# Kernel tuning notes

Hardware: AMD Instinct MI355X
Metric: run time of the kernel (lower is better)

## Reference

```python
import jax, jax.numpy as jnp
import numpy as np

N_CLASSES = 64
MAX_ITER = 50
EPS = 1e-4


def _sqdist(x, y):
    # squared euclidean distances [n, m]
    d = (x * x).sum(-1)[:, None] + (y * y).sum(-1)[None, :] - 2.0 * (x @ y.T)
    return jnp.maximum(d, 0.0)


def setup_inputs() -> dict:
    key = jax.random.key(0)
    k1, k2, k3 = jax.random.split(key, 3)
    return {
        "feat_s": jax.random.normal(k1, (1600, 1024), jnp.float32),
        "y_s": jax.random.randint(k2, (1600,), 0, N_CLASSES),
        "feat_q": jax.random.normal(k3, (4096, 1024), jnp.float32),
    }


def _prototypes(feat_s, y_s):
    sums = jax.ops.segment_sum(feat_s, y_s, num_segments=N_CLASSES)
    cnt = jax.ops.segment_sum(jnp.ones((feat_s.shape[0],), feat_s.dtype), y_s, num_segments=N_CLASSES)
    return sums / jnp.maximum(cnt, 1.0)[:, None]


def _affinity(feat):
    n = feat.shape[0]
    k = max(1, int(np.log2(n)))  # self-tuning neighborhood size
    dist = jnp.sqrt(_sqdist(feat, feat))
    _, nn_idx = jax.lax.top_k(-dist, k + 1)  # ascending distance order
    rows = jnp.arange(n)
    sigma = dist[rows, nn_idx[:, k]] + 1e-8  # k-th neighbor distance
    nbrs = nn_idx[:, 1:]  # [n, k], drop self
    w = jnp.exp(-jnp.take_along_axis(dist, nbrs, axis=1) / (sigma[:, None] * sigma[nbrs]))
    W = jnp.zeros((n, n), feat.dtype).at[rows[:, None], nbrs].set(w)
    W = (W + W.T) / 2.0
    D_inv = 1.0 / (W.sum(1) + 1e-8)
    return W, D_inv


def _mm_iterations(feat, prototypes, W, D_inv, lam):
    a = _sqdist(feat, prototypes)  # [n, C]
    coef = (lam * D_inv)[:, None]

    def step(y):
        return jax.nn.softmax(-a + coef * (W @ y), axis=1)

    y0 = jax.nn.softmax(-a, axis=1)

    def cond(s):
        y, y_new, i = s
        return (i < MAX_ITER) & (jnp.max(jnp.abs(y_new - y)) >= EPS)

    def body(s):
        y, y_new, i = s
        return (y_new, step(y_new), i + 1)

    y, _, _ = jax.lax.while_loop(cond, body, (y0, step(y0), 0))
    return y


def reference(feat_s, y_s, feat_q):
    protos = _prototypes(feat_s, y_s)
    W, D_inv = _affinity(feat_q)
    d2 = _sqdist(feat_q, protos).min(1)  # squared min distance to prototypes
    d = jnp.sqrt(d2)
    lam = jnp.exp(-d2 / (2.0 * jnp.median(d) ** 2 + 1e-8))
    y = _mm_iterations(feat_q, protos, W, D_inv, lam)
    return jnp.argmax(y, axis=1)
```

## Files before the change

kernel.cpp:

```cpp
#include <hip/hip_runtime.h>
#include <hip/hip_cooperative_groups.h>
#include <cfloat>
#include <cmath>

#define N_Q 4096
#define N_S 1600
#define DIM 1024
#define N_C 64
#define KNN 12
#define MAX_ITER 50
#define EPS_CONV 1e-4f
#define NBLK 256
#define ADJ_CAP 96
#define CHK 256
#define DPAD 40

typedef _Float16 h8 __attribute__((ext_vector_type(8)));
typedef float    f4 __attribute__((ext_vector_type(4)));

__device__ __forceinline__ float wave_max64(float v){
  #pragma unroll
  for (int o = 32; o; o >>= 1) v = fmaxf(v, __shfl_xor(v, o, 64));
  return v;
}
__device__ __forceinline__ float wave_sum64(float v){
  #pragma unroll
  for (int o = 32; o; o >>= 1) v += __shfl_xor(v, o, 64);
  return v;
}
__device__ __forceinline__ float wave_min64(float v){
  #pragma unroll
  for (int o = 32; o; o >>= 1) v = fminf(v, __shfl_xor(v, o, 64));
  return v;
}

__device__ __forceinline__ float aload(const float* p){
  return __hip_atomic_load(p, __ATOMIC_RELAXED, __HIP_MEMORY_SCOPE_AGENT);
}
__device__ __forceinline__ void astore(float* p, float v){
  __hip_atomic_store(p, v, __ATOMIC_RELAXED, __HIP_MEMORY_SCOPE_AGENT);
}
__device__ __forceinline__ int aloadi(const int* p){
  return __hip_atomic_load(p, __ATOMIC_RELAXED, __HIP_MEMORY_SCOPE_AGENT);
}
__device__ __forceinline__ void astorei(int* p, int v){
  __hip_atomic_store(p, v, __ATOMIC_RELAXED, __HIP_MEMORY_SCOPE_AGENT);
}
__device__ __forceinline__ unsigned long long aload64(const unsigned long long* p){
  return __hip_atomic_load(p, __ATOMIC_RELAXED, __HIP_MEMORY_SCOPE_AGENT);
}
__device__ __forceinline__ void astore64(unsigned long long* p, unsigned long long v){
  __hip_atomic_store(p, v, __ATOMIC_RELAXED, __HIP_MEMORY_SCOPE_AGENT);
}

__global__ __launch_bounds__(256) void setup_kernel(
    const float* __restrict__ fs, const int* __restrict__ ys,
    float* __restrict__ Pt, float* __restrict__ pn,
    const float* __restrict__ X, float* __restrict__ qn,
    _Float16* __restrict__ Xh, _Float16* __restrict__ Xl)
{
  __shared__ union {
    struct {
      int   list[N_S];
      int   pref[256];
      int   lcount;
      float red[256];
    } p;
    float red[256];
  } S;

  const int t = threadIdx.x;

  if (blockIdx.x < N_C){
    const int c = blockIdx.x;
    int loc[7]; int cnt = 0;
    const int base = t * 7;
    #pragma unroll
    for (int u = 0; u < 7; u++){
      const int i = base + u;
      if (i < N_S && ys[i] == c) loc[cnt++] = i;
    }
    S.p.pref[t] = cnt;
    __syncthreads();
    for (int off = 1; off < 256; off <<= 1){
      int v = (t >= off) ? S.p.pref[t - off] : 0;
      __syncthreads();
      S.p.pref[t] += v;
      __syncthreads();
    }
    const int start = S.p.pref[t] - cnt;
    for (int u = 0; u < cnt; u++) S.p.list[start + u] = loc[u];
    if (t == 255) S.p.lcount = S.p.pref[255];
    __syncthreads();

    const int n = S.p.lcount;
    float a0 = 0.f, a1 = 0.f, a2 = 0.f, a3 = 0.f;
    for (int m = 0; m < n; m++){
      const float* r = fs + (size_t)S.p.list[m] * DIM;
      a0 += r[t]; a1 += r[t + 256]; a2 += r[t + 512]; a3 += r[t + 768];
    }
    const float inv = 1.0f / fmaxf((float)n, 1.0f);
    const float v0 = a0*inv, v1 = a1*inv, v2 = a2*inv, v3 = a3*inv;
    Pt[(t      )*N_C + c] = v0;
    Pt[(t + 256)*N_C + c] = v1;
    Pt[(t + 512)*N_C + c] = v2;
    Pt[(t + 768)*N_C + c] = v3;
    S.p.red[t] = v0*v0 + v1*v1 + v2*v2 + v3*v3;
    __syncthreads();
    for (int o = 128; o; o >>= 1){ if (t < o) S.p.red[t] += S.p.red[t + o]; __syncthreads(); }
    if (t == 0) pn[c] = S.p.red[0];
  } else {
    const int i = blockIdx.x - N_C;
    const float* r = X + (size_t)i * DIM;
    const float v0 = r[t], v1 = r[t+256], v2 = r[t+512], v3 = r[t+768];
    const size_t b = (size_t)i * DIM;
    _Float16 h0 = (_Float16)v0, h1 = (_Float16)v1, h2 = (_Float16)v2, h3 = (_Float16)v3;
    Xh[b + t      ] = h0; Xl[b + t      ] = (_Float16)(v0 - (float)h0);
    Xh[b + t + 256] = h1; Xl[b + t + 256] = (_Float16)(v1 - (float)h1);
    Xh[b + t + 512] = h2; Xl[b + t + 512] = (_Float16)(v2 - (float)h2);
    Xh[b + t + 768] = h3; Xl[b + t + 768] = (_Float16)(v3 - (float)h3);
    S.red[t] = v0*v0 + v1*v1 + v2*v2 + v3*v3;
    __syncthreads();
    for (int o = 128; o; o >>= 1){ if (t < o) S.red[t] += S.red[t + o]; __syncthreads(); }
    if (t == 0) qn[i] = S.red[0];
  }
}

__global__ __launch_bounds__(256, 2) void dist_mfma(
    const _Float16* __restrict__ Xh, const _Float16* __restrict__ Xl,
    const float* __restrict__ qn, float* __restrict__ Dq)
{
  __shared__ __align__(16) _Float16 As[2][128][DPAD];
  __shared__ __align__(16) _Float16 Bs[2][256][DPAD];

  const int t = threadIdx.x, w = t >> 6, l = t & 63;
  const int lb  = blockIdx.x;
  const int xcd = lb & 7, k = lb >> 3;
  const int bxs = xcd * 2 + (k >> 5);
  const int bys = k & 31;
  const int bi0 = bys * 128, bj0 = bxs * 256;
  const int j0w = w * 64;
  const int fr = l & 15;
  const int kq = (l >> 4) * 8;

  const int arow = t >> 1;
  const int aseg = (t & 1) * 16;
  const int brow = t;

  f4 acc[8][4];
  #pragma unroll
  for (int a = 0; a < 8; a++)
    #pragma unroll
    for (int b = 0; b < 4; b++) acc[a][b] = (f4){0.f, 0.f, 0.f, 0.f};

  const size_t abase = (size_t)(bi0 + arow) * DIM + aseg;
  const size_t bbase = (size_t)(bj0 + brow) * DIM;

  #pragma unroll 1
  for (int k0 = 0; k0 < DIM; k0 += 32){
    h8 va0 = *(const h8*)(Xh + abase + k0);
    h8 va1 = *(const h8*)(Xh + abase + k0 + 8);
    h8 vb0 = *(const h8*)(Xl + abase + k0);
    h8 vb1 = *(const h8*)(Xl + abase + k0 + 8);
    h8 vc0 = *(const h8*)(Xh + bbase + k0);
    h8 vc1 = *(const h8*)(Xh + bbase + k0 + 8);
    h8 vc2 = *(const h8*)(Xh + bbase + k0 + 16);
    h8 vc3 = *(const h8*)(Xh + bbase + k0 + 24);
    h8 vd0 = *(const h8*)(Xl + bbase + k0);
    h8 vd1 = *(const h8*)(Xl + bbase + k0 + 8);
    h8 vd2 = *(const h8*)(Xl + bbase + k0 + 16);
    h8 vd3 = *(const h8*)(Xl + bbase + k0 + 24);
    __syncthreads();
    *(h8*)&As[0][arow][aseg    ] = va0;
    *(h8*)&As[0][arow][aseg + 8] = va1;
    *(h8*)&As[1][arow][aseg    ] = vb0;
    *(h8*)&As[1][arow][aseg + 8] = vb1;
    *(h8*)&Bs[0][brow][0 ] = vc0;
    *(h8*)&Bs[0][brow][8 ] = vc1;
    *(h8*)&Bs[0][brow][16] = vc2;
    *(h8*)&Bs[0][brow][24] = vc3;
    *(h8*)&Bs[1][brow][0 ] = vd0;
    *(h8*)&Bs[1][brow][8 ] = vd1;
    *(h8*)&Bs[1][brow][16] = vd2;
    *(h8*)&Bs[1][brow][24] = vd3;
    __syncthreads();

    h8 ah[8], al[8];
    #pragma unroll
    for (int sm = 0; sm < 8; sm++){
      ah[sm] = *(const h8*)&As[0][sm * 16 + fr][kq];
      al[sm] = *(const h8*)&As[1][sm * 16 + fr][kq];
    }
    #pragma unroll
    for (int sn = 0; sn < 4; sn++){
      h8 bh = *(const h8*)&Bs[0][j0w + sn * 16 + fr][kq];
      h8 bl = *(const h8*)&Bs[1][j0w + sn * 16 + fr][kq];
      #pragma unroll
      for (int sm = 0; sm < 8; sm++){
        acc[sm][sn] = __builtin_amdgcn_mfma_f32_16x16x32_f16(ah[sm], bh, acc[sm][sn], 0, 0, 0);
        acc[sm][sn] = __builtin_amdgcn_mfma_f32_16x16x32_f16(ah[sm], bl, acc[sm][sn], 0, 0, 0);
        acc[sm][sn] = __builtin_amdgcn_mfma_f32_16x16x32_f16(al[sm], bh, acc[sm][sn], 0, 0, 0);
      }
    }
  }

  const int cr = (l >> 4) * 4;
  const int cc = l & 15;
  #pragma unroll
  for (int sm = 0; sm < 8; sm++){
    #pragma unroll
    for (int r = 0; r < 4; r++){
      const int row = bi0 + sm * 16 + cr + r;
      const float qi = qn[row];
      float* dstrow = &Dq[(size_t)row * N_Q];
      #pragma unroll
      for (int sn = 0; sn < 4; sn++){
        const int col = bj0 + j0w + sn * 16 + cc;
        float d2 = qi + qn[col] - 2.0f * acc[sm][sn][r];
        dstrow[col] = sqrtf(fmaxf(d2, 0.f));
      }
    }
  }
}

__global__ __launch_bounds__(256) void topk_kernel(
    const float* __restrict__ Dq, int* __restrict__ nbr,
    float* __restrict__ dnbr, float* __restrict__ sigma)
{
  const int i = blockIdx.x, t = threadIdx.x;
  const int lane = t & 63, w = t >> 6;
  const float* row = Dq + (size_t)i * N_Q;
  float r[16];
  #pragma unroll
  for (int u = 0; u < 16; u++) r[u] = row[t + u * 256];

  __shared__ float cvf[4 * (KNN + 1)];
  __shared__ int   cif[4 * (KNN + 1)];

  float keepv = FLT_MAX; int keepi = 0x7fffffff;
  for (int s = 0; s < KNN + 1; s++){
    float best = FLT_MAX; int bj = 0x7fffffff;
    #pragma unroll
    for (int u = 0; u < 16; u++){
      float v = r[u];
      if (v < best){ best = v; bj = t + u * 256; }
    }
    #pragma unroll
    for (int o = 32; o; o >>= 1){
      float ov = __shfl_xor(best, o, 64); int oj = __shfl_xor(bj, o, 64);
      if (ov < best || (ov == best && oj < bj)){ best = ov; bj = oj; }
    }
    if (lane == s){ keepv = best; keepi = bj; }
    if ((bj & 255) == t) r[bj >> 8] = FLT_MAX;
  }
  if (lane < KNN + 1){ cvf[w * (KNN + 1) + lane] = keepv; cif[w * (KNN + 1) + lane] = keepi; }
  __syncthreads();

  if (w == 0){
    float mv = FLT_MAX; int mi = 0x7fffffff;
    if (lane < 4 * (KNN + 1)){ mv = cvf[lane]; mi = cif[lane]; }
    for (int s = 0; s < KNN + 1; s++){
      float best = mv; int bj = mi;
      #pragma unroll
      for (int o = 32; o; o >>= 1){
        float ov = __shfl_xor(best, o, 64); int oj = __shfl_xor(bj, o, 64);
        if (ov < best || (ov == best && oj < bj)){ best = ov; bj = oj; }
      }
      if (lane == 0){
        if (s >= 1){ nbr[i*KNN + s - 1] = bj; dnbr[i*KNN + s - 1] = best; }
        if (s == KNN) sigma[i] = best + 1e-8f;
      }
      if (mi == bj) mv = FLT_MAX;
    }
  }
}

__device__ __forceinline__ void gbar_leader(int* garr, int* gcnt, int* gen, int target){
  const int g = blockIdx.x >> 4;
  int old = __hip_atomic_fetch_add(&garr[g * 32], 1, __ATOMIC_RELAXED, __HIP_MEMORY_SCOPE_AGENT);
  if ((old & 15) == 15){
    int o2 = __hip_atomic_fetch_add(gcnt, 1, __ATOMIC_RELAXED, __HIP_MEMORY_SCOPE_AGENT);
    if ((o2 & 15) == 15)
      __hip_atomic_fetch_add(gen, 1, __ATOMIC_RELAXED, __HIP_MEMORY_SCOPE_AGENT);
  }
  while (__hip_atomic_load(gen, __ATOMIC_RELAXED, __HIP_MEMORY_SCOPE_AGENT) < target)
    __builtin_amdgcn_s_sleep(1);
}

__device__ __forceinline__ void pbar_wave0(
    unsigned long long* pslot, int ph, int* sdm, float* sdelta_sh, int lane)
{
  const int par = ph & 1;
  unsigned long long* base = pslot + (size_t)par * NBLK;
  if (lane == 0){
    int myd = sdm[par]; sdm[par] = 0;
    unsigned long long pack =
        ((unsigned long long)(unsigned int)myd << 32) | (unsigned int)ph;
    __builtin_amdgcn_s_waitcnt(0);
    astore64(&base[blockIdx.x], pack);
  }
  int mx;
  while (1){
    unsigned long long v0 = aload64(&base[lane      ]);
    unsigned long long v1 = aload64(&base[lane +  64]);
    unsigned long long v2 = aload64(&base[lane + 128]);
    unsigned long long v3 = aload64(&base[lane + 192]);
    int f0 = (int)(unsigned int)v0, f1 = (int)(unsigned int)v1;
    int f2 = (int)(unsigned int)v2, f3 = (int)(unsigned int)v3;
    int mn = f0 < f1 ? f0 : f1;
    mn = f2 < mn ? f2 : mn;
    mn = f3 < mn ? f3 : mn;
    if (__all(mn >= ph)){
      int d0 = (int)(v0 >> 32), d1 = (int)(v1 >> 32);
      int d2 = (int)(v2 >> 32), d3 = (int)(v3 >> 32);
      mx = d0 > d1 ? d0 : d1;
      mx = d2 > mx ? d2 : mx;
      mx = d3 > mx ? d3 : mx;
      break;
    }
    __builtin_amdgcn_s_sleep(1);
  }
  #pragma unroll
  for (int o = 32; o; o >>= 1){ int ox = __shfl_xor(mx, o, 64); mx = ox > mx ? ox : mx; }
  if (lane == 0) *sdelta_sh = __int_as_float(mx);
}

template<int K>
__device__ __forceinline__ void chunk_fma(
    const float* __restrict__ src, const int2* adj, int gbase, int lane,
    float& s0, float& s1, float& s2, float& s3,
    float& s4, float& s5, float& s6, float& s7)
{
  float yv[K][8], wv[K][8];
  #pragma unroll
  for (int g = 0; g < K; g++){
    #pragma unroll
    for (int u = 0; u < 8; u++){
      int2 a = adj[(gbase + g) * 8 + u];
      wv[g][u] = __int_as_float(a.y);
      yv[g][u] = aload(&src[a.x + lane]);
    }
  }
  #pragma unroll
  for (int g = 0; g < K; g++){
    s0 = fmaf(wv[g][0], yv[g][0], s0);
    s1 = fmaf(wv[g][1], yv[g][1], s1);
    s2 = fmaf(wv[g][2], yv[g][2], s2);
    s3 = fmaf(wv[g][3], yv[g][3], s3);
    s4 = fmaf(wv[g][4], yv[g][4], s4);
    s5 = fmaf(wv[g][5], yv[g][5], s5);
    s6 = fmaf(wv[g][6], yv[g][6], s6);
    s7 = fmaf(wv[g][7], yv[g][7], s7);
  }
}

__device__ __forceinline__ float spmv_row(
    const float* __restrict__ src, const int2* adj,
    const int* __restrict__ colA, const float* __restrict__ wA,
    int p0, int p1v, int lane)
{
  const int deg  = p1v - p0;
  const int ncap = deg < ADJ_CAP ? deg : ADJ_CAP;
  const int nfull = ncap & ~7;
  const int ng = nfull >> 3;
  float s0=0.f,s1=0.f,s2=0.f,s3=0.f,s4=0.f,s5=0.f,s6=0.f,s7=0.f;

  int g = 0;
  #pragma unroll 1
  for (; g + 4 <= ng; g += 4){
    chunk_fma<4>(src, adj, g, lane, s0,s1,s2,s3,s4,s5,s6,s7);
  }
  {
    const int left = ng - g;
    if (left == 3)      chunk_fma<3>(src, adj, g, lane, s0,s1,s2,s3,s4,s5,s6,s7);
    else if (left == 2) chunk_fma<2>(src, adj, g, lane, s0,s1,s2,s3,s4,s5,s6,s7);
    else if (left == 1) chunk_fma<1>(src, adj, g, lane, s0,s1,s2,s3,s4,s5,s6,s7);
  }

  if (deg > ADJ_CAP){
    int qg = p0 + ADJ_CAP;
    for (; qg + 8 <= p1v; qg += 8){
      s0 = fmaf(wA[qg    ], aload(&src[colA[qg    ] + lane]), s0);
      s1 = fmaf(wA[qg + 1], aload(&src[colA[qg + 1] + lane]), s1);
      s2 = fmaf(wA[qg + 2], aload(&src[colA[qg + 2] + lane]), s2);
      s3 = fmaf(wA[qg + 3], aload(&src[colA[qg + 3] + lane]), s3);
      s4 = fmaf(wA[qg + 4], aload(&src[colA[qg + 4] + lane]), s4);
      s5 = fmaf(wA[qg + 5], aload(&src[colA[qg + 5] + lane]), s5);
      s6 = fmaf(wA[qg + 6], aload(&src[colA[qg + 6] + lane]), s6);
      s7 = fmaf(wA[qg + 7], aload(&src[colA[qg + 7] + lane]), s7);
    }
    for (; qg < p1v; qg++)
      s0 = fmaf(wA[qg], aload(&src[colA[qg] + lane]), s0);
  } else {
    const int rem = deg - nfull;
    if (rem > 0){
      float yr[7], wr[7];
      #pragma unroll
      for (int u = 0; u < 7; u++){
        if (u < rem){
          int2 a = adj[nfull + u];
          wr[u] = __int_as_float(a.y);
          yr[u] = aload(&src[a.x + lane]);
        }
      }
      #pragma unroll
      for (int u = 0; u < 7; u++)
        if (u < rem) s0 = fmaf(wr[u], yr[u], s0);
    }
  }
  return ((s0+s1)+(s2+s3)) + ((s4+s5)+(s6+s7));
}

__global__ __launch_bounds__(1024, 4) void tail_loop(
    const float* __restrict__ Xq, const float* __restrict__ Pt,
    const float* __restrict__ pn, const float* __restrict__ qn,
    const int* __restrict__ nbr, const float* __restrict__ dnbr,
    const float* __restrict__ sigma,
    float* d2min, float* denom, float* wh,
    float* rowsum, int* indeg, int* rowptr, int* fillc,
    int* colA, float* wA, float* buf0, float* buf1,
    unsigned long long* pslot,
    int* gcnt, int* gen, int* garr, int* __restrict__ out)
{
  __shared__ int   sdm[2];
  __shared__ float sdelta;
  __shared__ union {
    float pchunk[CHK * N_C];
    struct {
      int   ipart[1024];
      int   hist[1024];
      float cand[4096];
      int   candn, b1s, b2s;
    } s;
  } U;
  __shared__ int2  adjL[16 * ADJ_CAP];

  const int tid  = threadIdx.x;
  const int lane = tid & 63;
  const int wv   = tid >> 6;
  const int row  = blockIdx.x * 16 + wv;
  if (tid == 0){ sdm[0] = 0; sdm[1] = 0; }

  const float* xr = Xq + (size_t)row * DIM;
  const f4*    xr4 = (const f4*)xr;
  float dp[8];
  #pragma unroll
  for (int u = 0; u < 8; u++) dp[u] = 0.f;

  for (int f0 = 0; f0 < DIM; f0 += CHK){
    const f4* srcv = (const f4*)(Pt + (size_t)f0 * N_C);
    f4* dstv = (f4*)U.pchunk;
    #pragma unroll
    for (int u = 0; u < 4; u++) dstv[tid + u * 1024] = srcv[tid + u * 1024];
    __syncthreads();
    #pragma unroll 1
    for (int f = 0; f < CHK; f += 8){
      const f4 xa = xr4[(f0 + f) >> 2];
      const f4 xb = xr4[((f0 + f) >> 2) + 1];
      const float* pc = U.pchunk + f * N_C + lane;
      dp[0] = fmaf(xa[0], pc[0      ], dp[0]);
      dp[1] = fmaf(xa[1], pc[N_C    ], dp[1]);
      dp[2] = fmaf(xa[2], pc[N_C * 2], dp[2]);
      dp[3] = fmaf(xa[3], pc[N_C * 3], dp[3]);
      dp[4] = fmaf(xb[0], pc[N_C * 4], dp[4]);
      dp[5] = fmaf(xb[1], pc[N_C * 5], dp[5]);
      dp[6] = fmaf(xb[2], pc[N_C * 6], dp[6]);
      dp[7] = fmaf(xb[3], pc[N_C * 7], dp[7]);
    }
    __syncthreads();
  }
  const float dot = ((dp[0]+dp[1])+(dp[2]+dp[3])) + ((dp[4]+dp[5])+(dp[6]+dp[7]));
  const float av  = fmaxf(qn[row] + pn[lane] - 2.0f * dot, 0.0f);
  const float d2m = wave_min64(av);
  if (lane == 0) astore(&d2min[row], d2m);

  const int e = blockIdx.x * 1024 + tid;
  if (e < N_Q * KNN){
    const int i = e / KNN;
    const int j = nbr[e];
    float wgt = 0.5f * expf(-dnbr[e] / (sigma[i] * sigma[j]));
    astore(&wh[e], wgt);
    atomicAdd(&rowsum[i], wgt);
    atomicAdd(&rowsum[j], wgt);
    atomicAdd(&indeg[j], 1);
  }

  __syncthreads();
  if (tid == 0) gbar_leader(garr, gcnt, gen, 1);
  __syncthreads();

  float xv = -av;
  float m = wave_max64(xv), ee = expf(xv - m), ss = wave_sum64(ee);
  float prev = ee / ss;
  astore(&buf0[row * N_C + lane], prev);

  if (blockIdx.x == 0){
    int* ipart = U.s.ipart;
    const int base = tid * 4;
    int c0 = aloadi(&indeg[base]),     c1 = aloadi(&indeg[base + 1]);
    int c2 = aloadi(&indeg[base + 2]), c3 = aloadi(&indeg[base + 3]);
    const int s4 = c0 + c1 + c2 + c3;
    ipart[tid] = s4;
    __syncthreads();
    for (int off = 1; off < 1024; off <<= 1){
      int v = (tid >= off) ? ipart[tid - off] : 0;
      __syncthreads();
      ipart[tid] += v;
      __syncthreads();
    }
    int run = ipart[tid] - s4;
    astorei(&rowptr[base    ], KNN * (base    ) + run); run += c0;
    astorei(&rowptr[base + 1], KNN * (base + 1) + run); run += c1;
    astorei(&rowptr[base + 2], KNN * (base + 2) + run); run += c2;
    astorei(&rowptr[base + 3], KNN * (base + 3) + run);
    if (tid == 1023) astorei(&rowptr[N_Q], KNN * N_Q + ipart[1023]);
  }
  if (blockIdx.x == 1){
    int*   hist = U.s.hist;
    float* cand = U.s.cand;
    const int base = tid * 4;
    float dv[4];
    #pragma unroll
    for (int u = 0; u < 4; u++) dv[u] = sqrtf(aload(&d2min[base + u]));
    float mn = fminf(fminf(dv[0], dv[1]), fminf(dv[2], dv[3]));
    float mx = fmaxf(fmaxf(dv[0], dv[1]), fmaxf(dv[2], dv[3]));
    mn = wave_min64(mn); mx = wave_max64(mx);
    if (lane == 0){ cand[wv] = mn; cand[wv + 16] = mx; }
    __syncthreads();
    if (tid == 0){
      float a = cand[0], b = cand[16];
      for (int k = 1; k < 16; k++){ a = fminf(a, cand[k]); b = fmaxf(b, cand[16 + k]); }
      cand[32] = a; cand[33] = b;
    }
    __syncthreads();
    mn = cand[32]; mx = cand[33];
    const float rng = mx - mn;
    const float scale = (rng > 0.f) ? (1024.0f / rng) : 0.f;
    hist[tid] = 0;
    __syncthreads();
    int bidx[4];
    #pragma unroll
    for (int u = 0; u < 4; u++){
      int b = (int)((dv[u] - mn) * scale);
      b = b < 0 ? 0 : (b > 1023 ? 1023 : b);
      bidx[u] = b;
      atomicAdd(&hist[b], 1);
    }
    __syncthreads();
    for (int off = 1; off < 1024; off <<= 1){
      int v = (tid >= off) ? hist[tid - off] : 0;
      __syncthreads();
      hist[tid] += v;
      __syncthreads();
    }
    if (hist[tid] >= 2048 && (tid == 0 || hist[tid - 1] < 2048)) U.s.b1s = tid;
    if (hist[tid] >= 2049 && (tid == 0 || hist[tid - 1] < 2049)) U.s.b2s = tid;
    if (tid == 0) U.s.candn = 0;
    __syncthreads();
    const int b1 = U.s.b1s, b2 = U.s.b2s;
    const int cntBefore = (b1 > 0) ? hist[b1 - 1] : 0;
    #pragma unroll
    for (int u = 0; u < 4; u++){
      if (bidx[u] >= b1 && bidx[u] <= b2){
        int pos = atomicAdd(&U.s.candn, 1);
        cand[pos] = dv[u];
      }
    }
    __syncthreads();
    const int mcnt = U.s.candn;
    int P = 2; while (P < mcnt) P <<= 1;
    for (int i2 = mcnt + tid; i2 < P; i2 += 1024) cand[i2] = FLT_MAX;
    __syncthreads();
    for (int k = 2; k <= P; k <<= 1){
      for (int st = k >> 1; st > 0; st >>= 1){
        for (int i2 = tid; i2 < P; i2 += 1024){
          int j2 = i2 ^ st;
          if (j2 > i2){
            float a2 = cand[i2], b3 = cand[j2];
            bool up = ((i2 & k) == 0);
            if (up ? (a2 > b3) : (a2 < b3)){ cand[i2] = b3; cand[j2] = a2; }
          }
        }
        __syncthreads();
      }
    }
    if (tid == 0){
      float v1 = cand[2047 - cntBefore], v2 = cand[2048 - cntBefore];
      float med = 0.5f * (v1 + v2);
      astore(denom, 2.0f * med * med + 1e-8f);
    }
  }

  __syncthreads();
  if (tid == 0) gbar_leader(garr, gcnt, gen, 2);
  __syncthreads();

  if (e < N_Q * KNN){
    const int i = e / KNN, tt = e % KNN;
    const int j = nbr[e];
    const float wgt = aload(&wh[e]);
    const int p = aloadi(&rowptr[i]) + tt;
    colA[p] = j * N_C; wA[p] = wgt;
    const int q = aloadi(&rowptr[j]) + KNN + atomicAdd(&fillc[j], 1);
    colA[q] = i * N_C; wA[q] = wgt;
  }
  const float cf = expf(-d2m / aload(denom)) / (aload(&rowsum[row]) + 1e-8f);
  const int p0  = aloadi(&rowptr[row]);
  const int p1v = aloadi(&rowptr[row + 1]);

  __builtin_amdgcn_fence(__ATOMIC_RELEASE, "agent");
  __syncthreads();
  if (tid == 0) gbar_leader(garr, gcnt, gen, 3);
  __syncthreads();
  __builtin_amdgcn_fence(__ATOMIC_ACQUIRE, "agent");

  {
    const int deg  = p1v - p0;
    const int ncap = deg < ADJ_CAP ? deg : ADJ_CAP;
    for (int u = lane; u < ncap; u += 64)
      adjL[wv * ADJ_CAP + u] = make_int2(colA[p0 + u], __float_as_int(wA[p0 + u]));
  }
  __syncthreads();
  const int2* adj = adjL + wv * ADJ_CAP;

  float cur;
  {
    float sum = spmv_row(buf0, adj, colA, wA, p0, p1v, lane);
    float xv2 = -av + cf * sum;
    float mm = wave_max64(xv2), e2 = expf(xv2 - mm), ss2 = wave_sum64(e2);
    cur = e2 / ss2;
    astore(&buf1[row * N_C + lane], cur);
  }
  float dm = wave_max64(fabsf(cur - prev));
  if (lane == 0) atomicMax(&sdm[1], __float_as_int(dm));
  __syncthreads();
  if (wv == 0) pbar_wave0(pslot, 1, sdm, &sdelta, lane);
  __syncthreads();
  float delta = sdelta;

  int par = 1;
  for (int t = 0;; t++){
    if (t >= MAX_ITER || delta < EPS_CONV) break;
    const float* src = par ? buf1 : buf0;
    float*       dst = par ? buf0 : buf1;
    float sum = spmv_row(src, adj, colA, wA, p0, p1v, lane);
    float xv2 = -av + cf * sum;
    float mm = wave_max64(xv2), e2 = expf(xv2 - mm), ss2 = wave_sum64(e2);
    float nxt = e2 / ss2;
    astore(&dst[row * N_C + lane], nxt);
    const int ph = t + 2;
    dm = wave_max64(fabsf(nxt - cur));
    if (lane == 0) atomicMax(&sdm[ph & 1], __float_as_int(dm));
    __syncthreads();
    if (wv == 0) pbar_wave0(pslot, ph, sdm, &sdelta, lane);
    __syncthreads();
    delta = sdelta;
    prev = cur; cur = nxt; par ^= 1;
  }

  float bv = prev; int bi = lane;
  #pragma unroll
  for (int o = 32; o; o >>= 1){
    float ov = __shfl_xor(bv, o, 64); int oi = __shfl_xor(bi, o, 64);
    if (ov > bv || (ov == bv && oi < bi)){ bv = ov; bi = oi; }
  }
  if (lane == 0) out[row] = bi;
}

extern "C" void kernel_launch(void* const* d_in, const int* in_sizes, int n_in,
                              void* d_out, int out_size, void* d_ws, size_t ws_size,
                              hipStream_t stream)
{
  const float* feat_s = (const float*)d_in[0];
  const int*   y_s    = (const int*)d_in[1];
  const float* feat_q = (const float*)d_in[2];
  int* out = (int*)d_out;

  char* wp = (char*)d_ws;
  auto alloc = [&](size_t bytes) -> char* {
    char* p = wp;
    wp += (bytes + 255) & ~(size_t)255;
    return p;
  };
  float*     Dq  = (float*)alloc((size_t)N_Q * N_Q * 4);
  _Float16*  Xh  = (_Float16*)alloc((size_t)N_Q * DIM * 2);
  _Float16*  Xl  = (_Float16*)alloc((size_t)N_Q * DIM * 2);
  float* Pt     = (float*)alloc((size_t)DIM * N_C * 4);
  float* pn     = (float*)alloc(N_C * 4);
  float* qn     = (float*)alloc(N_Q * 4);
  float* d2min  = (float*)alloc(N_Q * 4);
  float* denom  = (float*)alloc(256);
  int*   nbr    = (int*)alloc((size_t)N_Q * KNN * 4);
  float* dnbr   = (float*)alloc((size_t)N_Q * KNN * 4);
  float* sigma  = (float*)alloc(N_Q * 4);
  float* wh     = (float*)alloc((size_t)N_Q * KNN * 4);
  int*   rowptr = (int*)alloc((N_Q + 1) * 4);
  int*   colA   = (int*)alloc((size_t)2 * N_Q * KNN * 4);
  float* wA     = (float*)alloc((size_t)2 * N_Q * KNN * 4);
  float* buf0   = (float*)alloc((size_t)N_Q * N_C * 4);
  float* buf1   = (float*)alloc((size_t)N_Q * N_C * 4);
  const size_t zbytes = (size_t)N_Q*12 + 256 + 2048 + 2 * NBLK * 8;
  char*  zbase  = alloc(zbytes);
  float* rowsum = (float*)(zbase);
  int*   indeg  = (int*)(zbase + N_Q*4);
  int*   fillc  = (int*)(zbase + N_Q*8);
  int*   syncw  = (int*)(zbase + N_Q*12);
  int*   garr   = (int*)(zbase + N_Q*12 + 256);
  unsigned long long* pslot = (unsigned long long*)(zbase + N_Q*12 + 256 + 2048);

  hipMemsetAsync(zbase, 0, zbytes, stream);

  setup_kernel <<<N_Q + N_C, 256, 0, stream>>>(feat_s, y_s, Pt, pn, feat_q, qn, Xh, Xl);
  dist_mfma    <<<512, 256, 0, stream>>>(Xh, Xl, qn, Dq);
  topk_kernel  <<<N_Q, 256, 0, stream>>>(Dq, nbr, dnbr, sigma);

  int* gcnt = &syncw[0];
  int* gen  = &syncw[32];
  const float* Xq = feat_q;
  void* args[] = {&Xq, &Pt, &pn, &qn, &nbr, &dnbr, &sigma,
                  &d2min, &denom, &wh, &rowsum, &indeg, &rowptr, &fillc,
                  &colA, &wA, &buf0, &buf1, &pslot,
                  &gcnt, &gen, &garr, &out};
  hipLaunchCooperativeKernel((void*)tail_loop, dim3(NBLK), dim3(1024), args, 0, stream);
}
```

Before: 454.2 us.

## Move prototype distances and median out of cooperative tail kernel

Query-to-prototype distances move into a separate av_kernel launched before the pairwise distance GEMM, with results stored to a buffer. The median-based lambda denominator now runs in one extra block of topk_kernel using 256 threads, instead of block 1 of the cooperative tail kernel. The goal is to shorten the serial section before the tail kernel's first grid barrier and to shrink its shared memory. The cost is an extra kernel launch, a round trip of the distance matrix through global memory, and a slower per-thread median step with 16 elements per thread.

```diff
diff --git a/kernel.cpp b/kernel.cpp
--- a/kernel.cpp
+++ b/kernel.cpp
@@ -124,6 +124,53 @@
     for (int o = 128; o; o >>= 1){ if (t < o) S.red[t] += S.red[t + o]; __syncthreads(); }
     if (t == 0) qn[i] = S.red[0];
   }
+}
+
+__global__ __launch_bounds__(1024) void av_kernel(
+    const float* __restrict__ Xq, const float* __restrict__ Pt,
+    const float* __restrict__ pn, const float* __restrict__ qn,
+    float* __restrict__ avb, float* __restrict__ d2min)
+{
+  __shared__ float pchunk[CHK * N_C];
+
+  const int tid  = threadIdx.x;
+  const int lane = tid & 63;
+  const int wv   = tid >> 6;
+  const int row  = blockIdx.x * 16 + wv;
+
+  const float* xr = Xq + (size_t)row * DIM;
+  const f4*    xr4 = (const f4*)xr;
+  float dp[8];
+  #pragma unroll
+  for (int u = 0; u < 8; u++) dp[u] = 0.f;
+
+  for (int f0 = 0; f0 < DIM; f0 += CHK){
+    const f4* srcv = (const f4*)(Pt + (size_t)f0 * N_C);
+    f4* dstv = (f4*)pchunk;
+    #pragma unroll
+    for (int u = 0; u < 4; u++) dstv[tid + u * 1024] = srcv[tid + u * 1024];
+    __syncthreads();
+    #pragma unroll 1
+    for (int f = 0; f < CHK; f += 8){
+      const f4 xa = xr4[(f0 + f) >> 2];
+      const f4 xb = xr4[((f0 + f) >> 2) + 1];
+      const float* pc = pchunk + f * N_C + lane;
+      dp[0] = fmaf(xa[0], pc[0      ], dp[0]);
+      dp[1] = fmaf(xa[1], pc[N_C    ], dp[1]);
+      dp[2] = fmaf(xa[2], pc[N_C * 2], dp[2]);
+      dp[3] = fmaf(xa[3], pc[N_C * 3], dp[3]);
+      dp[4] = fmaf(xb[0], pc[N_C * 4], dp[4]);
+      dp[5] = fmaf(xb[1], pc[N_C * 5], dp[5]);
+      dp[6] = fmaf(xb[2], pc[N_C * 6], dp[6]);
+      dp[7] = fmaf(xb[3], pc[N_C * 7], dp[7]);
+    }
+    __syncthreads();
+  }
+  const float dot = ((dp[0]+dp[1])+(dp[2]+dp[3])) + ((dp[4]+dp[5])+(dp[6]+dp[7]));
+  const float av  = fmaxf(qn[row] + pn[lane] - 2.0f * dot, 0.0f);
+  avb[row * N_C + lane] = av;
+  const float d2m = wave_min64(av);
+  if (lane == 0) d2min[row] = d2m;
 }
 
 __global__ __launch_bounds__(256, 2) void dist_mfma(
@@ -225,52 +272,147 @@
 
 __global__ __launch_bounds__(256) void topk_kernel(
     const float* __restrict__ Dq, int* __restrict__ nbr,
-    float* __restrict__ dnbr, float* __restrict__ sigma)
-{
+    float* __restrict__ dnbr, float* __restrict__ sigma,
+    const float* __restrict__ d2min, float* __restrict__ denom)
+{
+  __shared__ int   hist[1024];
+  __shared__ float cand[4096];
+  __shared__ int   csum[256];
+  __shared__ int   candn, b1s, b2s;
+  __shared__ float cvf[4 * (KNN + 1)];
+  __shared__ int   cif[4 * (KNN + 1)];
+
   const int i = blockIdx.x, t = threadIdx.x;
   const int lane = t & 63, w = t >> 6;
-  const float* row = Dq + (size_t)i * N_Q;
-  float r[16];
-  #pragma unroll
-  for (int u = 0; u < 16; u++) r[u] = row[t + u * 256];
-
-  __shared__ float cvf[4 * (KNN + 1)];
-  __shared__ int   cif[4 * (KNN + 1)];
-
-  float keepv = FLT_MAX; int keepi = 0x7fffffff;
-  for (int s = 0; s < KNN + 1; s++){
-    float best = FLT_MAX; int bj = 0x7fffffff;
-    #pragma unroll
-    for (int u = 0; u < 16; u++){
-      float v = r[u];
-      if (v < best){ best = v; bj = t + u * 256; }
-    }
-    #pragma unroll
-    for (int o = 32; o; o >>= 1){
-      float ov = __shfl_xor(best, o, 64); int oj = __shfl_xor(bj, o, 64);
-      if (ov < best || (ov == best && oj < bj)){ best = ov; bj = oj; }
-    }
-    if (lane == s){ keepv = best; keepi = bj; }
-    if ((bj & 255) == t) r[bj >> 8] = FLT_MAX;
-  }
-  if (lane < KNN + 1){ cvf[w * (KNN + 1) + lane] = keepv; cif[w * (KNN + 1) + lane] = keepi; }
-  __syncthreads();
-
-  if (w == 0){
-    float mv = FLT_MAX; int mi = 0x7fffffff;
-    if (lane < 4 * (KNN + 1)){ mv = cvf[lane]; mi = cif[lane]; }
+
+  if (i < N_Q){
+    const float* row = Dq + (size_t)i * N_Q;
+    float r[16];
+    #pragma unroll
+    for (int u = 0; u < 16; u++) r[u] = row[t + u * 256];
+
+    float keepv = FLT_MAX; int keepi = 0x7fffffff;
     for (int s = 0; s < KNN + 1; s++){
-      float best = mv; int bj = mi;
+      float best = FLT_MAX; int bj = 0x7fffffff;
+      #pragma unroll
+      for (int u = 0; u < 16; u++){
+        float v = r[u];
+        if (v < best){ best = v; bj = t + u * 256; }
+      }
       #pragma unroll
       for (int o = 32; o; o >>= 1){
         float ov = __shfl_xor(best, o, 64); int oj = __shfl_xor(bj, o, 64);
         if (ov < best || (ov == best && oj < bj)){ best = ov; bj = oj; }
       }
-      if (lane == 0){
-        if (s >= 1){ nbr[i*KNN + s - 1] = bj; dnbr[i*KNN + s - 1] = best; }
-        if (s == KNN) sigma[i] = best + 1e-8f;
+      if (lane == s){ keepv = best; keepi = bj; }
+      if ((bj & 255) == t) r[bj >> 8] = FLT_MAX;
+    }
+    if (lane < KNN + 1){ cvf[w * (KNN + 1) + lane] = keepv; cif[w * (KNN + 1) + lane] = keepi; }
+    __syncthreads();
+
+    if (w == 0){
+      float mv = FLT_MAX; int mi = 0x7fffffff;
+      if (lane < 4 * (KNN + 1)){ mv = cvf[lane]; mi = cif[lane]; }
+      for (int s = 0; s < KNN + 1; s++){
+        float best = mv; int bj = mi;
+        #pragma unroll
+        for (int o = 32; o; o >>= 1){
+          float ov = __shfl_xor(best, o, 64); int oj = __shfl_xor(bj, o, 64);
+          if (ov < best || (ov == best && oj < bj)){ best = ov; bj = oj; }
+        }
+        if (lane == 0){
+          if (s >= 1){ nbr[i*KNN + s - 1] = bj; dnbr[i*KNN + s - 1] = best; }
+          if (s == KNN) sigma[i] = best + 1e-8f;
+        }
+        if (mi == bj) mv = FLT_MAX;
       }
-      if (mi == bj) mv = FLT_MAX;
+    }
+  } else {
+    float dv[16];
+    int   bidx[16];
+    #pragma unroll
+    for (int u = 0; u < 16; u++) dv[u] = sqrtf(aload(&d2min[t * 16 + u]));
+    float mn = dv[0], mx = dv[0];
+    #pragma unroll
+    for (int u = 1; u < 16; u++){ mn = fminf(mn, dv[u]); mx = fmaxf(mx, dv[u]); }
+    mn = wave_min64(mn); mx = wave_max64(mx);
+    if (lane == 0){ cand[w] = mn; cand[w + 4] = mx; }
+    __syncthreads();
+    if (t == 0){
+      float a = cand[0], b = cand[4];
+      for (int k = 1; k < 4; k++){ a = fminf(a, cand[k]); b = fmaxf(b, cand[4 + k]); }
+      cand[8] = a; cand[9] = b;
+    }
+    __syncthreads();
+    mn = cand[8]; mx = cand[9];
+    const float rng = mx - mn;
+    const float scale = (rng > 0.f) ? (1024.0f / rng) : 0.f;
+    #pragma unroll
+    for (int u = 0; u < 4; u++) hist[t * 4 + u] = 0;
+    __syncthreads();
+    #pragma unroll
+    for (int u = 0; u < 16; u++){
+      int b = (int)((dv[u] - mn) * scale);
+      b = b < 0 ? 0 : (b > 1023 ? 1023 : b);
+      bidx[u] = b;
+      atomicAdd(&hist[b], 1);
+    }
+    __syncthreads();
+    int h0 = hist[t*4], h1 = hist[t*4+1], h2 = hist[t*4+2], h3 = hist[t*4+3];
+    const int s4 = h0 + h1 + h2 + h3;
+    csum[t] = s4;
+    __syncthreads();
+    for (int off = 1; off < 256; off <<= 1){
+      int v = (t >= off) ? csum[t - off] : 0;
+      __syncthreads();
+      csum[t] += v;
+      __syncthreads();
+    }
+    int run = csum[t] - s4;
+    hist[t*4    ] = run + h0;
+    hist[t*4 + 1] = run + h0 + h1;
+    hist[t*4 + 2] = run + h0 + h1 + h2;
+    hist[t*4 + 3] = run + h0 + h1 + h2 + h3;
+    __syncthreads();
+    #pragma unroll
+    for (int u = 0; u < 4; u++){
+      const int b = t * 4 + u;
+      if (hist[b] >= 2048 && (b == 0 || hist[b - 1] < 2048)) b1s = b;
+      if (hist[b] >= 2049 && (b == 0 || hist[b - 1] < 2049)) b2s = b;
+    }
+    if (t == 0) candn = 0;
+    __syncthreads();
+    const int b1 = b1s, b2 = b2s;
+    const int cntBefore = (b1 > 0) ? hist[b1 - 1] : 0;
+    #pragma unroll
+    for (int u = 0; u < 16; u++){
+      if (bidx[u] >= b1 && bidx[u] <= b2){
+        int pos = atomicAdd(&candn, 1);
+        cand[pos] = dv[u];
+      }
+    }
+    __syncthreads();
+    const int mcnt = candn;
+    int P = 2; while (P < mcnt) P <<= 1;
+    for (int i2 = mcnt + t; i2 < P; i2 += 256) cand[i2] = FLT_MAX;
+    __syncthreads();
+    for (int k = 2; k <= P; k <<= 1){
+      for (int st = k >> 1; st > 0; st >>= 1){
+        for (int i2 = t; i2 < P; i2 += 256){
+          int j2 = i2 ^ st;
+          if (j2 > i2){
+            float a2 = cand[i2], b3 = cand[j2];
+            bool up = ((i2 & k) == 0);
+            if (up ? (a2 > b3) : (a2 < b3)){ cand[i2] = b3; cand[j2] = a2; }
+          }
+        }
+        __syncthreads();
+      }
+    }
+    if (t == 0){
+      float v1 = cand[2047 - cntBefore], v2 = cand[2048 - cntBefore];
+      float med = 0.5f * (v1 + v2);
+      astore(denom, 2.0f * med * med + 1e-8f);
     }
   }
 }
@@ -412,11 +554,10 @@
 }
 
 __global__ __launch_bounds__(1024, 4) void tail_loop(
-    const float* __restrict__ Xq, const float* __restrict__ Pt,
-    const float* __restrict__ pn, const float* __restrict__ qn,
+    const float* __restrict__ avb,
     const int* __restrict__ nbr, const float* __restrict__ dnbr,
     const float* __restrict__ sigma,
-    float* d2min, float* denom, float* wh,
+    float* denom, float* wh,
     float* rowsum, int* indeg, int* rowptr, int* fillc,
     int* colA, float* wA, float* buf0, float* buf1,
     unsigned long long* pslot,
@@ -424,15 +565,7 @@
 {
   __shared__ int   sdm[2];
   __shared__ float sdelta;
-  __shared__ union {
-    float pchunk[CHK * N_C];
-    struct {
-      int   ipart[1024];
-      int   hist[1024];
-      float cand[4096];
-      int   candn, b1s, b2s;
-    } s;
-  } U;
+  __shared__ int   ipart[1024];
   __shared__ int2  adjL[16 * ADJ_CAP];
 
   const int tid  = threadIdx.x;
@@ -441,38 +574,8 @@
   const int row  = blockIdx.x * 16 + wv;
   if (tid == 0){ sdm[0] = 0; sdm[1] = 0; }
 
-  const float* xr = Xq + (size_t)row * DIM;
-  const f4*    xr4 = (const f4*)xr;
-  float dp[8];
-  #pragma unroll
-  for (int u = 0; u < 8; u++) dp[u] = 0.f;
-
-  for (int f0 = 0; f0 < DIM; f0 += CHK){
-    const f4* srcv = (const f4*)(Pt + (size_t)f0 * N_C);
-    f4* dstv = (f4*)U.pchunk;
-    #pragma unroll
-    for (int u = 0; u < 4; u++) dstv[tid + u * 1024] = srcv[tid + u * 1024];
-    __syncthreads();
-    #pragma unroll 1
-    for (int f = 0; f < CHK; f += 8){
-      const f4 xa = xr4[(f0 + f) >> 2];
-      const f4 xb = xr4[((f0 + f) >> 2) + 1];
-      const float* pc = U.pchunk + f * N_C + lane;
-      dp[0] = fmaf(xa[0], pc[0      ], dp[0]);
-      dp[1] = fmaf(xa[1], pc[N_C    ], dp[1]);
-      dp[2] = fmaf(xa[2], pc[N_C * 2], dp[2]);
-      dp[3] = fmaf(xa[3], pc[N_C * 3], dp[3]);
-      dp[4] = fmaf(xb[0], pc[N_C * 4], dp[4]);
-      dp[5] = fmaf(xb[1], pc[N_C * 5], dp[5]);
-      dp[6] = fmaf(xb[2], pc[N_C * 6], dp[6]);
-      dp[7] = fmaf(xb[3], pc[N_C * 7], dp[7]);
-    }
-    __syncthreads();
-  }
-  const float dot = ((dp[0]+dp[1])+(dp[2]+dp[3])) + ((dp[4]+dp[5])+(dp[6]+dp[7]));
-  const float av  = fmaxf(qn[row] + pn[lane] - 2.0f * dot, 0.0f);
+  const float av  = avb[row * N_C + lane];
   const float d2m = wave_min64(av);
-  if (lane == 0) astore(&d2min[row], d2m);
 
   const int e = blockIdx.x * 1024 + tid;
   if (e < N_Q * KNN){
@@ -495,7 +598,6 @@
   astore(&buf0[row * N_C + lane], prev);
 
   if (blockIdx.x == 0){
-    int* ipart = U.s.ipart;
     const int base = tid * 4;
     int c0 = aloadi(&indeg[base]),     c1 = aloadi(&indeg[base + 1]);
     int c2 = aloadi(&indeg[base + 2]), c3 = aloadi(&indeg[base + 3]);
@@ -514,81 +616,6 @@
     astorei(&rowptr[base + 2], KNN * (base + 2) + run); run += c2;
     astorei(&rowptr[base + 3], KNN * (base + 3) + run);
     if (tid == 1023) astorei(&rowptr[N_Q], KNN * N_Q + ipart[1023]);
-  }
-  if (blockIdx.x == 1){
-    int*   hist = U.s.hist;
-    float* cand = U.s.cand;
-    const int base = tid * 4;
-    float dv[4];
-    #pragma unroll
-    for (int u = 0; u < 4; u++) dv[u] = sqrtf(aload(&d2min[base + u]));
-    float mn = fminf(fminf(dv[0], dv[1]), fminf(dv[2], dv[3]));
-    float mx = fmaxf(fmaxf(dv[0], dv[1]), fmaxf(dv[2], dv[3]));
-    mn = wave_min64(mn); mx = wave_max64(mx);
-    if (lane == 0){ cand[wv] = mn; cand[wv + 16] = mx; }
-    __syncthreads();
-    if (tid == 0){
-      float a = cand[0], b = cand[16];
-      for (int k = 1; k < 16; k++){ a = fminf(a, cand[k]); b = fmaxf(b, cand[16 + k]); }
-      cand[32] = a; cand[33] = b;
-    }
-    __syncthreads();
-    mn = cand[32]; mx = cand[33];
-    const float rng = mx - mn;
-    const float scale = (rng > 0.f) ? (1024.0f / rng) : 0.f;
-    hist[tid] = 0;
-    __syncthreads();
-    int bidx[4];
-    #pragma unroll
-    for (int u = 0; u < 4; u++){
-      int b = (int)((dv[u] - mn) * scale);
-      b = b < 0 ? 0 : (b > 1023 ? 1023 : b);
-      bidx[u] = b;
-      atomicAdd(&hist[b], 1);
-    }
-    __syncthreads();
-    for (int off = 1; off < 1024; off <<= 1){
-      int v = (tid >= off) ? hist[tid - off] : 0;
-      __syncthreads();
-      hist[tid] += v;
-      __syncthreads();
-    }
-    if (hist[tid] >= 2048 && (tid == 0 || hist[tid - 1] < 2048)) U.s.b1s = tid;
-    if (hist[tid] >= 2049 && (tid == 0 || hist[tid - 1] < 2049)) U.s.b2s = tid;
-    if (tid == 0) U.s.candn = 0;
-    __syncthreads();
-    const int b1 = U.s.b1s, b2 = U.s.b2s;
-    const int cntBefore = (b1 > 0) ? hist[b1 - 1] : 0;
-    #pragma unroll
-    for (int u = 0; u < 4; u++){
-      if (bidx[u] >= b1 && bidx[u] <= b2){
-        int pos = atomicAdd(&U.s.candn, 1);
-        cand[pos] = dv[u];
-      }
-    }
-    __syncthreads();
-    const int mcnt = U.s.candn;
-    int P = 2; while (P < mcnt) P <<= 1;
-    for (int i2 = mcnt + tid; i2 < P; i2 += 1024) cand[i2] = FLT_MAX;
-    __syncthreads();
-    for (int k = 2; k <= P; k <<= 1){
-      for (int st = k >> 1; st > 0; st >>= 1){
-        for (int i2 = tid; i2 < P; i2 += 1024){
-          int j2 = i2 ^ st;
-          if (j2 > i2){
-            float a2 = cand[i2], b3 = cand[j2];
-            bool up = ((i2 & k) == 0);
-            if (up ? (a2 > b3) : (a2 < b3)){ cand[i2] = b3; cand[j2] = a2; }
-          }
-        }
-        __syncthreads();
-      }
-    }
-    if (tid == 0){
-      float v1 = cand[2047 - cntBefore], v2 = cand[2048 - cntBefore];
-      float med = 0.5f * (v1 + v2);
-      astore(denom, 2.0f * med * med + 1e-8f);
-    }
   }
 
   __syncthreads();
@@ -688,6 +715,7 @@
   float* Pt     = (float*)alloc((size_t)DIM * N_C * 4);
   float* pn     = (float*)alloc(N_C * 4);
   float* qn     = (float*)alloc(N_Q * 4);
+  float* avb    = (float*)alloc((size_t)N_Q * N_C * 4);
   float* d2min  = (float*)alloc(N_Q * 4);
   float* denom  = (float*)alloc(256);
   int*   nbr    = (int*)alloc((size_t)N_Q * KNN * 4);
@@ -711,14 +739,14 @@
   hipMemsetAsync(zbase, 0, zbytes, stream);
 
   setup_kernel <<<N_Q + N_C, 256, 0, stream>>>(feat_s, y_s, Pt, pn, feat_q, qn, Xh, Xl);
+  av_kernel    <<<NBLK, 1024, 0, stream>>>(feat_q, Pt, pn, qn, avb, d2min);
   dist_mfma    <<<512, 256, 0, stream>>>(Xh, Xl, qn, Dq);
-  topk_kernel  <<<N_Q, 256, 0, stream>>>(Dq, nbr, dnbr, sigma);
+  topk_kernel  <<<N_Q + 1, 256, 0, stream>>>(Dq, nbr, dnbr, sigma, d2min, denom);
 
   int* gcnt = &syncw[0];
   int* gen  = &syncw[32];
-  const float* Xq = feat_q;
-  void* args[] = {&Xq, &Pt, &pn, &qn, &nbr, &dnbr, &sigma,
-                  &d2min, &denom, &wh, &rowsum, &indeg, &rowptr, &fillc,
+  void* args[] = {&avb, &nbr, &dnbr, &sigma,
+                  &denom, &wh, &rowsum, &indeg, &rowptr, &fillc,
                   &colA, &wA, &buf0, &buf1, &pslot,
                   &gcnt, &gen, &garr, &out};
   hipLaunchCooperativeKernel((void*)tail_loop, dim3(NBLK), dim3(1024), args, 0, stream);
```

Measured after the change: 464.5 us. +2.3%, slower.
